# Optimization experiments

Measured on AMD Instinct MI355X. Metric: run time of the kernel, lower is better.

The kernel has to match this reference:

```python
import jax, jax.numpy as jnp
import numpy as np

T = 4096
V = 88   # visible_dim
H = 512  # hidden_dim
R = 512  # rnn_hidden_dim
REG_FACTOR = 0.2
GIBBS_STEPS = 20
EPS = 1e-6


def setup_inputs() -> dict:
    key = jax.random.key(0)
    ks = jax.random.split(key, 8)
    scale = 1.0 / np.sqrt(H)
    return {
        "visible": (jax.random.uniform(ks[0], (T, V)) < 0.5).astype(jnp.float32),
        "rand_h": jax.random.uniform(ks[1], (T - 1, GIBBS_STEPS, H), dtype=jnp.float32),
        "rand_v": jax.random.uniform(ks[2], (T - 1, GIBBS_STEPS, V), dtype=jnp.float32),
        "w": jax.random.normal(ks[3], (H, V), dtype=jnp.float32) * scale,
        "wuu": jax.random.normal(ks[4], (R, R), dtype=jnp.float32) * scale,
        "wuv": jax.random.normal(ks[5], (V, R), dtype=jnp.float32) * scale,
        "wuh": jax.random.normal(ks[6], (H, R), dtype=jnp.float32) * scale,
        "wvu": jax.random.normal(ks[7], (R, V), dtype=jnp.float32) * scale,
        "bv": jnp.zeros((V,), jnp.float32),
        "bh": jnp.zeros((H,), jnp.float32),
        "bu": jnp.zeros((R,), jnp.float32),
        "u0": jnp.zeros((R,), jnp.float32),
    }


def reference(visible, rand_h, rand_v, w, wuu, wuv, wuh, wvu, bv, bh, bu, u0):
    time_steps = visible.shape[0]
    v_seq = visible[1:]  # v_t for t = 1..T-1, shape [T-1, V]

    # RNN state depends only on data, not on Gibbs samples -> single scan.
    def u_step(u_prev, v_t):
        u_new = jnp.tanh(wvu @ v_t + wuu @ u_prev + bu)
        return u_new, u_prev  # emit u_{t-1} (bias conditioning state)

    _, u_prev = jax.lax.scan(u_step, u0, v_seq)  # [T-1, R]

    # Per-timestep RBM biases (F.linear(u, W, b) = u @ W.T + b).
    bh_t = u_prev @ wuh.T + bh  # [T-1, H]
    bv_t = u_prev @ wuv.T + bv  # [T-1, V]

    # 20 Gibbs steps, batched over all time steps at once.
    def gibbs_step(v, rands):
        rh, rv = rands  # [T-1, H], [T-1, V]
        p_h = jax.nn.sigmoid(v @ w.T + bh_t)
        h = jax.nn.relu(jnp.sign(p_h - rh))         # Bernoulli sample
        p_v = jax.nn.sigmoid(h @ w + bv_t)
        v_new = jax.nn.relu(jnp.sign(p_v - rv))
        return v_new, None

    neg, _ = jax.lax.scan(
        gibbs_step, v_seq,
        (jnp.swapaxes(rand_h, 0, 1), jnp.swapaxes(rand_v, 0, 1)),
    )  # negative samples [T-1, V]

    # Cross-entropy between data and sigmoid(bv_t), summed then /time_steps.
    y_t = jax.nn.sigmoid(bv_t)
    total_cost = jnp.sum(
        -v_seq * jnp.log(EPS + y_t) - (1.0 - v_seq) * jnp.log(EPS + 1.0 - y_t)
    ) / time_steps

    reg_term = (jnp.linalg.norm(wuv) + jnp.linalg.norm(wuh)) * REG_FACTOR
    total_cost = total_cost + reg_term

    mse = jnp.mean(jnp.abs(v_seq - neg), axis=1)  # per-timestep, [T-1]
    return total_cost, mse, reg_term
```

## Files before the change

kernel.cpp:

```cpp
#include <hip/hip_runtime.h>
#include <cstdint>
#include <cstddef>

#define T4096 4096
#define TM1 4095
#define NV 88
#define NH 512
#define NR 512
#define GS 20
#define EPSV 1e-6f

#define U_OFF 0
#define AB_OFF 2096640
#define BV_OFF 4193280
#define SC_OFF 4553640

__device__ __forceinline__ unsigned int agent_load_u32(const unsigned int* p) {
  return __hip_atomic_load(p, __ATOMIC_RELAXED, __HIP_MEMORY_SCOPE_AGENT);
}
__device__ __forceinline__ void agent_store_f32(float* p, float v) {
  __hip_atomic_store(p, v, __ATOMIC_RELAXED, __HIP_MEMORY_SCOPE_AGENT);
}
__device__ __forceinline__ float sigmoidf_(float x) {
  return 1.0f / (1.0f + expf(-x));
}

__device__ __forceinline__ void store_sc0(float* p, float v) {
  asm volatile("global_store_dword %0, %1, off sc0" :: "v"(p), "v"(v) : "memory");
}
__device__ __forceinline__ unsigned load_sc0(const unsigned* p) {
  unsigned r;
  asm volatile("global_load_dword %0, %1, off sc0\n\ts_waitcnt vmcnt(0)"
               : "=v"(r) : "v"(p) : "memory");
  return r;
}
__device__ __forceinline__ void store_sys_f32(float* p, float v) {
  asm volatile("global_store_dword %0, %1, off sc0 sc1" :: "v"(p), "v"(v) : "memory");
}
__device__ __forceinline__ void store_sys_u32(unsigned* p, unsigned v) {
  asm volatile("global_store_dword %0, %1, off sc0 sc1" :: "v"(p), "v"(v) : "memory");
}
__device__ __forceinline__ unsigned load_sys_u32(const unsigned* p) {
  unsigned r;
  asm volatile("global_load_dword %0, %1, off sc0 sc1\n\ts_waitcnt vmcnt(0)"
               : "=v"(r) : "v"(p) : "memory");
  return r;
}
__device__ __forceinline__ float load_sys_f32(const float* p) {
  unsigned r;
  asm volatile("global_load_dword %0, %1, off sc0 sc1\n\ts_waitcnt vmcnt(0)"
               : "=v"(r) : "v"(p) : "memory");
  return __uint_as_float(r);
}

__device__ __forceinline__ unsigned poll_nd_sc0(const unsigned* p,
                                                unsigned& s1, unsigned& s2,
                                                unsigned& s3, unsigned& s4) {
  unsigned rA;
  asm volatile(
    "v_mov_b32 %0, -1\n\t"
    "global_load_dword %1, %5, off sc0\n\t"
    "global_load_dword %2, %5, off sc0\n\t"
    "global_load_dword %3, %5, off sc0\n\t"
    "global_load_dword %4, %5, off sc0\n\t"
    "Lr%=:\n\t"
    "s_waitcnt vmcnt(3)\n\t"
    "v_cmp_ne_u32 vcc, -1, %1\n\t"
    "v_cndmask_b32 %0, %0, %1, vcc\n\t"
    "v_cmp_eq_u32 vcc, -1, %0\n\t"
    "s_cbranch_vccz Le%=\n\t"
    "global_load_dword %1, %5, off sc0\n\t"
    "s_waitcnt vmcnt(3)\n\t"
    "v_cmp_ne_u32 vcc, -1, %2\n\t"
    "v_cndmask_b32 %0, %0, %2, vcc\n\t"
    "v_cmp_eq_u32 vcc, -1, %0\n\t"
    "s_cbranch_vccz Le%=\n\t"
    "global_load_dword %2, %5, off sc0\n\t"
    "s_waitcnt vmcnt(3)\n\t"
    "v_cmp_ne_u32 vcc, -1, %3\n\t"
    "v_cndmask_b32 %0, %0, %3, vcc\n\t"
    "v_cmp_eq_u32 vcc, -1, %0\n\t"
    "s_cbranch_vccz Le%=\n\t"
    "global_load_dword %3, %5, off sc0\n\t"
    "s_waitcnt vmcnt(3)\n\t"
    "v_cmp_ne_u32 vcc, -1, %4\n\t"
    "v_cndmask_b32 %0, %0, %4, vcc\n\t"
    "v_cmp_eq_u32 vcc, -1, %0\n\t"
    "s_cbranch_vccz Le%=\n\t"
    "global_load_dword %4, %5, off sc0\n\t"
    "s_branch Lr%=\n\t"
    "Le%=:\n\t"
    : "=&v"(rA), "+v"(s1), "+v"(s2), "+v"(s3), "+v"(s4)
    : "v"(p) : "vcc", "memory");
  return rA;
}
__device__ __forceinline__ unsigned poll_nd_sys(const unsigned* p,
                                                unsigned& s1, unsigned& s2,
                                                unsigned& s3, unsigned& s4) {
  unsigned rA;
  asm volatile(
    "v_mov_b32 %0, -1\n\t"
    "global_load_dword %1, %5, off sc0 sc1\n\t"
    "global_load_dword %2, %5, off sc0 sc1\n\t"
    "global_load_dword %3, %5, off sc0 sc1\n\t"
    "global_load_dword %4, %5, off sc0 sc1\n\t"
    "Lq%=:\n\t"
    "s_waitcnt vmcnt(3)\n\t"
    "v_cmp_ne_u32 vcc, -1, %1\n\t"
    "v_cndmask_b32 %0, %0, %1, vcc\n\t"
    "v_cmp_eq_u32 vcc, -1, %0\n\t"
    "s_cbranch_vccz Lf%=\n\t"
    "global_load_dword %1, %5, off sc0 sc1\n\t"
    "s_waitcnt vmcnt(3)\n\t"
    "v_cmp_ne_u32 vcc, -1, %2\n\t"
    "v_cndmask_b32 %0, %0, %2, vcc\n\t"
    "v_cmp_eq_u32 vcc, -1, %0\n\t"
    "s_cbranch_vccz Lf%=\n\t"
    "global_load_dword %2, %5, off sc0 sc1\n\t"
    "s_waitcnt vmcnt(3)\n\t"
    "v_cmp_ne_u32 vcc, -1, %3\n\t"
    "v_cndmask_b32 %0, %0, %3, vcc\n\t"
    "v_cmp_eq_u32 vcc, -1, %0\n\t"
    "s_cbranch_vccz Lf%=\n\t"
    "global_load_dword %3, %5, off sc0 sc1\n\t"
    "s_waitcnt vmcnt(3)\n\t"
    "v_cmp_ne_u32 vcc, -1, %4\n\t"
    "v_cndmask_b32 %0, %0, %4, vcc\n\t"
    "v_cmp_eq_u32 vcc, -1, %0\n\t"
    "s_cbranch_vccz Lf%=\n\t"
    "global_load_dword %4, %5, off sc0 sc1\n\t"
    "s_branch Lq%=\n\t"
    "Lf%=:\n\t"
    : "=&v"(rA), "+v"(s1), "+v"(s2), "+v"(s3), "+v"(s4)
    : "v"(p) : "vcc", "memory");
  return rA;
}

__global__ __launch_bounds__(256) void k_a(const float* __restrict__ visible,
                                           const float* __restrict__ wvu,
                                           const float* __restrict__ bu,
                                           float* __restrict__ A) {
  __shared__ float vbuf[NV * 8];
  const int tid = threadIdx.x;
  const int t0 = blockIdx.x * 8;
  for (int idx = tid; idx < NV * 8; idx += 256) {
    int j = idx / NV, v = idx - j * NV;
    int t = t0 + j;
    vbuf[v * 8 + j] = (t < TM1) ? visible[(size_t)(t + 1) * NV + v] : 0.f;
  }
  __syncthreads();
  for (int rr = 0; rr < 2; rr++) {
    int r = tid + rr * 256;
    float b0 = bu[r];
    float acc[8];
#pragma unroll
    for (int j = 0; j < 8; j++) acc[j] = b0;
    const float* wr = wvu + (size_t)r * NV;
    for (int v = 0; v < NV; v++) {
      float wv = wr[v];
#pragma unroll
      for (int j = 0; j < 8; j++) acc[j] = fmaf(wv, vbuf[v * 8 + j], acc[j]);
    }
#pragma unroll
    for (int j = 0; j < 8; j++) {
      int t = t0 + j;
      if (t < TM1) A[(size_t)t * NR + r] = acc[j];
    }
  }
}

__global__ __launch_bounds__(256) void k_r(const float* __restrict__ wuv,
                                           const float* __restrict__ wuh,
                                           float* __restrict__ sc) {
  size_t stride = (size_t)gridDim.x * 256;
  size_t gid = (size_t)blockIdx.x * 256 + threadIdx.x;
  float s1 = 0.f, s2 = 0.f;
  for (size_t i = gid; i < (size_t)NV * NR; i += stride) { float x = wuv[i]; s1 = fmaf(x, x, s1); }
  for (size_t i = gid; i < (size_t)NH * NR; i += stride) { float x = wuh[i]; s2 = fmaf(x, x, s2); }
  for (int off = 32; off > 0; off >>= 1) {
    s1 += __shfl_down(s1, off, 64);
    s2 += __shfl_down(s2, off, 64);
  }
  if ((threadIdx.x & 63) == 0) {
    atomicAdd(&sc[1], s1);
    atomicAdd(&sc[2], s2);
  }
}

__global__ __launch_bounds__(512, 2) void k_u11(const float* __restrict__ wuu,
                                                float* A,
                                                const float* __restrict__ u0,
                                                float* __restrict__ U,
                                                unsigned* __restrict__ ub,
                                                const float* __restrict__ visible,
                                                const float* __restrict__ w,
                                                const float* __restrict__ rand_h,
                                                const float* __restrict__ rand_v,
                                                const float* __restrict__ wuh,
                                                const float* __restrict__ wuv,
                                                const float* __restrict__ bh,
                                                const float* __restrict__ bv,
                                                float* __restrict__ out) {
  __shared__ int s_slot;
  __shared__ int s_fast;
  __shared__ int s_cid;
  __shared__ float red2[256];
  __shared__ __align__(16) union {
    struct { float u_buf[NR]; float partials[2][1024]; } p;
    struct { float bht[8 * NH]; float bvt[8 * NV]; float uT[NR * 10]; } b;
    struct { float bht[8 * NH]; float bvt[8 * NV]; float vlds[NV * 10]; float hlds[NH * 10]; } g;
  } sh;
  const int tid = threadIdx.x;
  unsigned* claimc = ub + 8;
  unsigned* winner = ub + 16;
  unsigned* hs     = ub + 17;
  unsigned* vd     = ub + 33;
  unsigned* flags  = ub + 40;

  if (tid == 0) {
    unsigned xcd;
    asm volatile("s_getreg_b32 %0, hwreg(HW_REG_XCC_ID, 0, 4)" : "=s"(xcd));
    xcd &= 7u;
    unsigned c = atomicAdd(&claimc[xcd], 1u);
    int slot = -1;
    if (c < 4u) {
      if (c == 3u) atomicCAS(winner, 0xFFFFFFFFu, xcd);
      unsigned wnr;
      do { wnr = agent_load_u32(winner); } while (wnr == 0xFFFFFFFFu);
      if (wnr == xcd) slot = (int)c;
    }
    s_slot = slot;
  }
  __syncthreads();
  const int slot = s_slot;

  if (slot < 0) {
    if (tid == 0) s_cid = (int)atomicAdd(&ub[48], 1u);
    __syncthreads();
    const int cid = s_cid;
    if (cid >= 256) return;
    float ce = 0.f;
    for (int half = 0; half < 2; half++) {
      const int c = cid * 2 + half;
      const int t0 = c * 8;
      const int nt = min(8, TM1 - t0);
      unsigned need = (unsigned)((t0 + nt - 1 + 15) & ~15);
      if (need > 4080u) need = 4095u;
      if (tid == 0) {
        for (;;) {
          unsigned mn = 0xFFFFFFFFu;
          for (int i = 0; i < 8; i++) { unsigned f = load_sys_u32(&flags[i]); if (f < mn) mn = f; }
          if (mn >= need) break;
          __builtin_amdgcn_s_sleep(32);
        }
      }
      __syncthreads();
      for (int idx = tid; idx < 8 * NR; idx += 512) {
        int tt = idx >> 9, k = idx & 511;
        int t = t0 + tt;
        float v = 0.f;
        if (tt < nt) v = (t == 0) ? u0[k] : load_sys_f32(&A[(size_t)(t - 1) * NR + k]);
        sh.b.uT[k * 10 + tt] = v;
      }
      __syncthreads();
      {
        const int h = tid;
        const bool hasv = tid < NV;
        float acc1[8], accv[8];
#pragma unroll
        for (int i = 0; i < 8; i++) acc1[i] = accv[i] = 0.f;
        const float* w1p = wuh + (size_t)h * NR;
        const float* wvp = wuv + (size_t)(hasv ? tid : 0) * NR;
        for (int k = 0; k < NR; k++) {
          float u8[8];
#pragma unroll
          for (int q = 0; q < 2; q++) *(float4*)(u8 + 4 * q) = *(const float4*)(sh.b.uT + k * 10 + 4 * q);
          float a = w1p[k];
          float cc = hasv ? wvp[k] : 0.f;
#pragma unroll
          for (int i = 0; i < 8; i++) {
            acc1[i] = fmaf(a, u8[i], acc1[i]);
            accv[i] = fmaf(cc, u8[i], accv[i]);
          }
        }
        float bh1 = bh[h];
#pragma unroll
        for (int i = 0; i < 8; i++)
          if (i < nt) sh.b.bht[i * NH + h] = acc1[i] + bh1;
        if (hasv) {
          float bvv = bv[tid];
          for (int i = 0; i < nt; i++) {
            float x = accv[i] + bvv;
            sh.b.bvt[i * NV + tid] = x;
            float y = sigmoidf_(x);
            float vs = visible[(size_t)(t0 + i + 1) * NV + tid];
            ce += -vs * logf(EPSV + y) - (1.f - vs) * logf(EPSV + 1.f - y);
          }
        }
      }
      __syncthreads();
      for (int idx = tid; idx < NV * 8; idx += 512) {
        int j = idx / NV, v = idx - j * NV;
        sh.g.vlds[v * 10 + j] = (j < nt) ? visible[(size_t)(t0 + j + 1) * NV + v] : 0.f;
      }
      __syncthreads();
      const int h1 = tid;
      const int tg = tid >> 5, vg = tid & 31;
      const int v0 = vg * 4;
      const bool bact = (vg < 22) && (tg < 8);
      for (int k = 0; k < GS; k++) {
        {
          float acc1[8];
#pragma unroll
          for (int i = 0; i < 8; i++) acc1[i] = 0.f;
          const float* w1p = w + (size_t)h1 * NV;
          for (int v = 0; v < NV; v++) {
            float vv[8];
#pragma unroll
            for (int q = 0; q < 2; q++) *(float4*)(vv + 4 * q) = *(const float4*)(sh.g.vlds + v * 10 + 4 * q);
            float a = w1p[v];
#pragma unroll
            for (int i = 0; i < 8; i++) acc1[i] = fmaf(a, vv[i], acc1[i]);
          }
#pragma unroll
          for (int i = 0; i < 8; i++) {
            if (i < nt) {
              size_t t = (size_t)(t0 + i);
              float x1 = acc1[i] + sh.g.bht[i * NH + h1];
              float p1 = sigmoidf_(x1);
              float r1 = rand_h[(t * GS + k) * NH + h1];
              sh.g.hlds[h1 * 10 + i] = (p1 > r1) ? 1.f : 0.f;
            }
          }
        }
        __syncthreads();
        if (bact && tg < nt) {
          float acc[4] = {0.f, 0.f, 0.f, 0.f};
#pragma unroll 4
          for (int h = 0; h < NH; h++) {
            float hv = sh.g.hlds[h * 10 + tg];
            float4 w4 = *(const float4*)(w + (size_t)h * NV + v0);
            acc[0] = fmaf(hv, w4.x, acc[0]);
            acc[1] = fmaf(hv, w4.y, acc[1]);
            acc[2] = fmaf(hv, w4.z, acc[2]);
            acc[3] = fmaf(hv, w4.w, acc[3]);
          }
          size_t t = (size_t)(t0 + tg);
#pragma unroll
          for (int i = 0; i < 4; i++) {
            int v = v0 + i;
            float x = acc[i] + sh.g.bvt[tg * NV + v];
            float p = sigmoidf_(x);
            float r = rand_v[(t * GS + k) * NV + v];
            sh.g.vlds[v * 10 + tg] = (p > r) ? 1.f : 0.f;
          }
        }
        __syncthreads();
      }
      if (tid < nt) {
        float s = 0.f;
        for (int v = 0; v < NV; v++) {
          float vs = visible[(size_t)(t0 + tid + 1) * NV + v];
          s += fabsf(vs - sh.g.vlds[v * 10 + tid]);
        }
        out[1 + t0 + tid] = s / 88.f;
      }
      __syncthreads();
    }
    if (tid < 256) red2[tid] = ce;
    __syncthreads();
    for (int s = 128; s > 0; s >>= 1) {
      if (tid < s) red2[tid] += red2[tid + s];
      __syncthreads();
    }
    if (tid == 0) atomicAdd((float*)ub, red2[0]);
    return;
  }

  if (tid == 0) {
    int fast = 1;
    for (int round = 0; round < 4 && fast; ++round) {
      unsigned* hw = hs + round * 4;
      store_sc0((float*)&hw[slot], 0.0f);
      for (int o = 0; o < 4; ++o) {
        if (o == slot) continue;
        int ok = 0;
        for (int it = 0; it < 300; ++it) {
          if (load_sc0(&hw[o]) != 0xFFFFFFFFu) { ok = 1; break; }
        }
        if (!ok) fast = 0;
      }
    }
    __hip_atomic_store(&vd[slot], (unsigned)(fast ? 1 : 0),
                       __ATOMIC_RELAXED, __HIP_MEMORY_SCOPE_AGENT);
    for (int o = 0; o < 4; ++o) {
      unsigned v;
      do { v = agent_load_u32(&vd[o]); } while (v == 0xFFFFFFFFu);
      if (v != 1u) fast = 0;
    }
    s_fast = fast;
  }
  __syncthreads();
  const int fast = s_fast;

  const int lane = tid & 63;
  const int kc   = tid >> 6;
  const int r0   = slot * 128;
  const bool is_red = (kc >> 1) == slot;
  const int s_row = ((kc & 1) << 6) + lane;
  const int fid = slot * 2 + (kc & 1);
  float* ubw = sh.p.u_buf + kc * 64;

  float WregA[64], WregB[64];
  {
    const float* wra = wuu + (size_t)(r0 + lane) * NR + kc * 64;
    const float* wrb = wuu + (size_t)(r0 + lane + 64) * NR + kc * 64;
#pragma unroll
    for (int i = 0; i < 16; i++) {
      ((float4*)WregA)[i] = ((const float4*)wra)[i];
      ((float4*)WregB)[i] = ((const float4*)wrb)[i];
    }
  }
#pragma unroll
  for (int i = 0; i < 64; i++) asm volatile("" : "+v"(WregA[i]));
#pragma unroll
  for (int i = 0; i < 64; i++) asm volatile("" : "+v"(WregB[i]));

  float val = 0.f, a_cur = 0.f;
  if (is_red) {
    agent_store_f32(&U[r0 + s_row], u0[r0 + s_row]);
    a_cur = A[r0 + s_row];
  }
  unsigned ps1 = 0, ps2 = 0, ps3 = 0, ps4 = 0;
  __syncthreads();

#define KU_STEP(T_, UVAL_) do {                                                \
    ubw[lane] = (UVAL_);                                                       \
    float acc0 = 0.f, acc1 = 0.f;                                              \
    _Pragma("unroll")                                                          \
    for (int i = 0; i < 64; i += 4) {                                          \
      float4 uv = *(const float4*)(ubw + i);                                   \
      acc0 = fmaf(WregA[i],     uv.x, acc0);                                   \
      acc1 = fmaf(WregB[i],     uv.x, acc1);                                   \
      acc0 = fmaf(WregA[i + 1], uv.y, acc0);                                   \
      acc1 = fmaf(WregB[i + 1], uv.y, acc1);                                   \
      acc0 = fmaf(WregA[i + 2], uv.z, acc0);                                   \
      acc1 = fmaf(WregB[i + 2], uv.z, acc1);                                   \
      acc0 = fmaf(WregA[i + 3], uv.w, acc0);                                   \
      acc1 = fmaf(WregB[i + 3], uv.w, acc1);                                   \
    }                                                                          \
    float* pb = sh.p.partials[(T_) & 1];                                       \
    pb[kc * 128 + lane] = acc0;                                                \
    pb[kc * 128 + lane + 64] = acc1;                                           \
    __syncthreads();                                                           \
    if (is_red) {                                                              \
      float s = a_cur;                                                         \
      _Pragma("unroll")                                                        \
      for (int kk = 0; kk < 8; kk++) s += pb[kk * 128 + s_row];                \
      val = tanhf(s);                                                          \
      if (fast) store_sc0(&U[(size_t)(T_) * NR + r0 + s_row], val);            \
      else      agent_store_f32(&U[(size_t)(T_) * NR + r0 + s_row], val);      \
      store_sys_f32(&A[(size_t)((T_) - 1) * NR + r0 + s_row], val);            \
      a_cur = A[(size_t)(T_) * NR + r0 + s_row];    \
      if (((T_) & 15) == 0) {                                                  \
        asm volatile("s_waitcnt vmcnt(0)" ::: "memory");                       \
        if (lane == 0) store_sys_u32(&flags[fid], (unsigned)(T_));             \
      }                                                                        \
    }                                                                          \
  } while (0)

  KU_STEP(1, u0[kc * 64 + lane]);
  for (int t = 2; t <= TM1 - 1; t++) {
    float u_val;
    if (is_red) {
      u_val = val;
    } else {
      const unsigned* p = (const unsigned*)(U + (size_t)(t - 1) * NR) + kc * 64 + lane;
      unsigned wv = fast ? poll_nd_sc0(p, ps1, ps2, ps3, ps4)
                         : poll_nd_sys(p, ps1, ps2, ps3, ps4);
      u_val = __uint_as_float(wv);
    }
    KU_STEP(t, u_val);
  }
#undef KU_STEP
  if (is_red) {
    asm volatile("s_waitcnt vmcnt(0)" ::: "memory");
    if (lane == 0) store_sys_u32(&flags[fid], 4095u);
  }
}

__global__ void k_f(const float* __restrict__ sc, float* __restrict__ out) {
  float reg = 0.2f * (sqrtf(sc[1]) + sqrtf(sc[2]));
  out[0] = sc[0] / 4096.f + reg;
  out[4096] = reg;
}

extern "C" void kernel_launch(void* const* d_in, const int* in_sizes, int n_in,
                              void* d_out, int out_size, void* d_ws, size_t ws_size,
                              hipStream_t stream) {
  const float* visible = (const float*)d_in[0];
  const float* rand_h  = (const float*)d_in[1];
  const float* rand_v  = (const float*)d_in[2];
  const float* w       = (const float*)d_in[3];
  const float* wuu     = (const float*)d_in[4];
  const float* wuv     = (const float*)d_in[5];
  const float* wuh     = (const float*)d_in[6];
  const float* wvu     = (const float*)d_in[7];
  const float* bv      = (const float*)d_in[8];
  const float* bh      = (const float*)d_in[9];
  const float* bu      = (const float*)d_in[10];
  const float* u0      = (const float*)d_in[11];
  float* out = (float*)d_out;
  float* ws = (float*)d_ws;

  float* Uarr = ws + U_OFF;
  float* Aarr = ws + AB_OFF;
  float* sc   = ws + SC_OFF;
  unsigned* ub = (unsigned*)sc;

  hipMemsetAsync(Uarr, 0xFF, (size_t)TM1 * NR * sizeof(float), stream);
  hipMemsetAsync(sc, 0, 64, stream);
  hipMemsetAsync((char*)sc + 64, 0xFF, 96, stream);
  hipMemsetAsync((char*)sc + 160, 0, 64, stream);

  k_a<<<512, 256, 0, stream>>>(visible, wvu, bu, Aarr);
  k_r<<<64, 256, 0, stream>>>(wuv, wuh, sc);
  k_u11<<<260, 512, 0, stream>>>(wuu, Aarr, u0, Uarr, ub,
                                 visible, w, rand_h, rand_v,
                                 wuh, wuv, bh, bv, out);
  k_f<<<1, 1, 0, stream>>>(sc, out);
}
```

Measured before the change: 5.777 ms.

## Make consumer blocks loop over dynamic chunks and coarsen producer progress flags

Consumer blocks no longer take two fixed chunks each. They now loop, atomically claiming 8-timestep chunks from a shared counter until all 512 are done, and reduce the cross-entropy per chunk. The grid shrinks to 256 blocks, and a large shared-memory pad forces fewer resident blocks per CU, presumably so the recurrent producer blocks are not starved. Producers publish progress flags every 32 steps instead of every 16, and the U-state loads become vectorized dwordx4 system-coherent loads with a padded stride-20 transpose in LDS. Coarser flags reduce producer stores but make consumers wait longer before they can start each chunk.

```diff
diff --git a/kernel.cpp b/kernel.cpp
--- a/kernel.cpp
+++ b/kernel.cpp
@@ -9,10 +9,10 @@
 #define NR 512
 #define GS 20
 #define EPSV 1e-6f
+#define NCHUNK 512
 
 #define U_OFF 0
 #define AB_OFF 2096640
-#define BV_OFF 4193280
 #define SC_OFF 4553640
 
 __device__ __forceinline__ unsigned int agent_load_u32(const unsigned int* p) {
@@ -46,11 +46,12 @@
                : "=v"(r) : "v"(p) : "memory");
   return r;
 }
-__device__ __forceinline__ float load_sys_f32(const float* p) {
-  unsigned r;
-  asm volatile("global_load_dword %0, %1, off sc0 sc1\n\ts_waitcnt vmcnt(0)"
-               : "=v"(r) : "v"(p) : "memory");
-  return __uint_as_float(r);
+__device__ __forceinline__ void load_sys_f32x4x2(const float* p, float4& a, float4& b) {
+  asm volatile("global_load_dwordx4 %0, %2, off sc0 sc1\n\t"
+               "global_load_dwordx4 %1, %3, off sc0 sc1\n\t"
+               "s_waitcnt vmcnt(0)"
+               : "=&v"(a), "=&v"(b)
+               : "v"(p), "v"(p + 4) : "memory");
 }
 
 __device__ __forceinline__ unsigned poll_nd_sc0(const unsigned* p,
@@ -187,7 +188,7 @@
   }
 }
 
-__global__ __launch_bounds__(512, 2) void k_u11(const float* __restrict__ wuu,
+__global__ __launch_bounds__(512, 2) void k_u12(const float* __restrict__ wuu,
                                                 float* A,
                                                 const float* __restrict__ u0,
                                                 float* __restrict__ U,
@@ -207,8 +208,9 @@
   __shared__ float red2[256];
   __shared__ __align__(16) union {
     struct { float u_buf[NR]; float partials[2][1024]; } p;
-    struct { float bht[8 * NH]; float bvt[8 * NV]; float uT[NR * 10]; } b;
-    struct { float bht[8 * NH]; float bvt[8 * NV]; float vlds[NV * 10]; float hlds[NH * 10]; } g;
+    struct { float bht[8 * NH]; float bvt[8 * NV]; float uT[NR * 20]; } b;
+    struct { float bht[8 * NH]; float bvt[8 * NV]; float vlds[NV * 10]; float hlds[NH * 20]; } g;
+    float occupancy_pad[21000];
   } sh;
   const int tid = threadIdx.x;
   unsigned* claimc = ub + 8;
@@ -235,34 +237,55 @@
   const int slot = s_slot;
 
   if (slot < 0) {
-    if (tid == 0) s_cid = (int)atomicAdd(&ub[48], 1u);
-    __syncthreads();
-    const int cid = s_cid;
-    if (cid >= 256) return;
-    float ce = 0.f;
-    for (int half = 0; half < 2; half++) {
-      const int c = cid * 2 + half;
-      const int t0 = c * 8;
-      const int nt = min(8, TM1 - t0);
-      unsigned need = (unsigned)((t0 + nt - 1 + 15) & ~15);
-      if (need > 4080u) need = 4095u;
+    const int h1 = tid;
+    const int tg = tid >> 5, vg = tid & 31;
+    const int v0 = vg * 4;
+    const bool bact = (vg < 22) && (tg < 8);
+    for (;;) {
+      if (tid == 0) s_cid = (int)atomicAdd(&ub[48], 1u);
+      __syncthreads();
+      const int c = s_cid;
+      if (c >= NCHUNK) break;
+      const int t0c = c * 8;
+      const int nt = min(8, TM1 - t0c);
+      unsigned need = (unsigned)((t0c + nt - 1 + 31) & ~31);
+      if (need > 4064u) need = 4095u;
       if (tid == 0) {
         for (;;) {
           unsigned mn = 0xFFFFFFFFu;
           for (int i = 0; i < 8; i++) { unsigned f = load_sys_u32(&flags[i]); if (f < mn) mn = f; }
           if (mn >= need) break;
-          __builtin_amdgcn_s_sleep(32);
-        }
-      }
-      __syncthreads();
-      for (int idx = tid; idx < 8 * NR; idx += 512) {
-        int tt = idx >> 9, k = idx & 511;
-        int t = t0 + tt;
-        float v = 0.f;
-        if (tt < nt) v = (t == 0) ? u0[k] : load_sys_f32(&A[(size_t)(t - 1) * NR + k]);
-        sh.b.uT[k * 10 + tt] = v;
-      }
-      __syncthreads();
+          __builtin_amdgcn_s_sleep(64);
+        }
+      }
+      __syncthreads();
+      {
+        const int tt = tid >> 6, kq = tid & 63;
+        const int t = t0c + tt;
+        float4 va, vb;
+        if (tt < nt) {
+          if (t == 0) {
+            va = *(const float4*)(u0 + kq * 8);
+            vb = *(const float4*)(u0 + kq * 8 + 4);
+          } else {
+            load_sys_f32x4x2(&A[(size_t)(t - 1) * NR + kq * 8], va, vb);
+          }
+        } else {
+          va.x = va.y = va.z = va.w = 0.f;
+          vb.x = vb.y = vb.z = vb.w = 0.f;
+        }
+        const int k0 = kq * 8;
+        sh.b.uT[(k0 + 0) * 20 + tt] = va.x;
+        sh.b.uT[(k0 + 1) * 20 + tt] = va.y;
+        sh.b.uT[(k0 + 2) * 20 + tt] = va.z;
+        sh.b.uT[(k0 + 3) * 20 + tt] = va.w;
+        sh.b.uT[(k0 + 4) * 20 + tt] = vb.x;
+        sh.b.uT[(k0 + 5) * 20 + tt] = vb.y;
+        sh.b.uT[(k0 + 6) * 20 + tt] = vb.z;
+        sh.b.uT[(k0 + 7) * 20 + tt] = vb.w;
+      }
+      __syncthreads();
+      float ce = 0.f;
       {
         const int h = tid;
         const bool hasv = tid < NV;
@@ -274,7 +297,7 @@
         for (int k = 0; k < NR; k++) {
           float u8[8];
 #pragma unroll
-          for (int q = 0; q < 2; q++) *(float4*)(u8 + 4 * q) = *(const float4*)(sh.b.uT + k * 10 + 4 * q);
+          for (int q = 0; q < 2; q++) *(float4*)(u8 + 4 * q) = *(const float4*)(sh.b.uT + k * 20 + 4 * q);
           float a = w1p[k];
           float cc = hasv ? wvp[k] : 0.f;
 #pragma unroll
@@ -293,7 +316,7 @@
             float x = accv[i] + bvv;
             sh.b.bvt[i * NV + tid] = x;
             float y = sigmoidf_(x);
-            float vs = visible[(size_t)(t0 + i + 1) * NV + tid];
+            float vs = visible[(size_t)(t0c + i + 1) * NV + tid];
             ce += -vs * logf(EPSV + y) - (1.f - vs) * logf(EPSV + 1.f - y);
           }
         }
@@ -301,13 +324,9 @@
       __syncthreads();
       for (int idx = tid; idx < NV * 8; idx += 512) {
         int j = idx / NV, v = idx - j * NV;
-        sh.g.vlds[v * 10 + j] = (j < nt) ? visible[(size_t)(t0 + j + 1) * NV + v] : 0.f;
-      }
-      __syncthreads();
-      const int h1 = tid;
-      const int tg = tid >> 5, vg = tid & 31;
-      const int v0 = vg * 4;
-      const bool bact = (vg < 22) && (tg < 8);
+        sh.g.vlds[v * 10 + j] = (j < nt) ? visible[(size_t)(t0c + j + 1) * NV + v] : 0.f;
+      }
+      __syncthreads();
       for (int k = 0; k < GS; k++) {
         {
           float acc1[8];
@@ -325,11 +344,11 @@
 #pragma unroll
           for (int i = 0; i < 8; i++) {
             if (i < nt) {
-              size_t t = (size_t)(t0 + i);
+              size_t t = (size_t)(t0c + i);
               float x1 = acc1[i] + sh.g.bht[i * NH + h1];
               float p1 = sigmoidf_(x1);
               float r1 = rand_h[(t * GS + k) * NH + h1];
-              sh.g.hlds[h1 * 10 + i] = (p1 > r1) ? 1.f : 0.f;
+              sh.g.hlds[h1 * 20 + i] = (p1 > r1) ? 1.f : 0.f;
             }
           }
         }
@@ -338,14 +357,14 @@
           float acc[4] = {0.f, 0.f, 0.f, 0.f};
 #pragma unroll 4
           for (int h = 0; h < NH; h++) {
-            float hv = sh.g.hlds[h * 10 + tg];
+            float hv = sh.g.hlds[h * 20 + tg];
             float4 w4 = *(const float4*)(w + (size_t)h * NV + v0);
             acc[0] = fmaf(hv, w4.x, acc[0]);
             acc[1] = fmaf(hv, w4.y, acc[1]);
             acc[2] = fmaf(hv, w4.z, acc[2]);
             acc[3] = fmaf(hv, w4.w, acc[3]);
           }
-          size_t t = (size_t)(t0 + tg);
+          size_t t = (size_t)(t0c + tg);
 #pragma unroll
           for (int i = 0; i < 4; i++) {
             int v = v0 + i;
@@ -360,20 +379,20 @@
       if (tid < nt) {
         float s = 0.f;
         for (int v = 0; v < NV; v++) {
-          float vs = visible[(size_t)(t0 + tid + 1) * NV + v];
+          float vs = visible[(size_t)(t0c + tid + 1) * NV + v];
           s += fabsf(vs - sh.g.vlds[v * 10 + tid]);
         }
-        out[1 + t0 + tid] = s / 88.f;
-      }
-      __syncthreads();
-    }
-    if (tid < 256) red2[tid] = ce;
-    __syncthreads();
-    for (int s = 128; s > 0; s >>= 1) {
-      if (tid < s) red2[tid] += red2[tid + s];
-      __syncthreads();
-    }
-    if (tid == 0) atomicAdd((float*)ub, red2[0]);
+        out[1 + t0c + tid] = s / 88.f;
+      }
+      if (tid < 256) red2[tid] = ce;
+      __syncthreads();
+      for (int s = 128; s > 0; s >>= 1) {
+        if (tid < s) red2[tid] += red2[tid + s];
+        __syncthreads();
+      }
+      if (tid == 0) atomicAdd((float*)ub, red2[0]);
+      __syncthreads();
+    }
     return;
   }
 
@@ -462,7 +481,7 @@
       else      agent_store_f32(&U[(size_t)(T_) * NR + r0 + s_row], val);      \
       store_sys_f32(&A[(size_t)((T_) - 1) * NR + r0 + s_row], val);            \
       a_cur = A[(size_t)(T_) * NR + r0 + s_row];    \
-      if (((T_) & 15) == 0) {                                                  \
+      if (((T_) & 31) == 0) {                                                  \
         asm volatile("s_waitcnt vmcnt(0)" ::: "memory");                       \
         if (lane == 0) store_sys_u32(&flags[fid], (unsigned)(T_));             \
       }                                                                        \
@@ -525,7 +544,7 @@
 
   k_a<<<512, 256, 0, stream>>>(visible, wvu, bu, Aarr);
   k_r<<<64, 256, 0, stream>>>(wuv, wuh, sc);
-  k_u11<<<260, 512, 0, stream>>>(wuu, Aarr, u0, Uarr, ub,
+  k_u12<<<256, 512, 0, stream>>>(wuu, Aarr, u0, Uarr, ub,
                                  visible, w, rand_h, rand_v,
                                  wuh, wuv, bh, bv, out);
   k_f<<<1, 1, 0, stream>>>(sc, out);
```

Result: faster. 5.253 ms (-9.1%).
